# Optimization experiments

Hardware: AMD Instinct MI355X
Metric: run time of the kernel (lower is better)

## Reference

```python
import jax, jax.numpy as jnp
import numpy as np

EMBED = 1024
HEADS = 16
HEAD_DIM = EMBED // HEADS


def setup_inputs() -> dict:
    key = jax.random.key(0)
    ks = jax.random.split(key, 6)
    s = 1.0 / np.sqrt(EMBED)
    return {
        "x": jax.random.normal(ks[0], (2, 2048, EMBED), dtype=jnp.float32),
        "Wq": jax.random.normal(ks[1], (EMBED, EMBED), dtype=jnp.float32) * s,
        "Wk": jax.random.normal(ks[2], (EMBED, EMBED), dtype=jnp.float32) * s,
        "Wv": jax.random.normal(ks[3], (EMBED, EMBED), dtype=jnp.float32) * s,
        "Wfc": jax.random.normal(ks[4], (EMBED, EMBED), dtype=jnp.float32) * s,
        "bfc": jnp.zeros((EMBED,), dtype=jnp.float32),
    }


def reference(x, Wq, Wk, Wv, Wfc, bfc):
    # x: (N, L, E). Linear(E,E,bias=False) applies y = x @ W.T (torch convention).
    N, L, E = x.shape
    q = (x @ Wq.T).reshape(N, L, HEADS, HEAD_DIM)
    k = (x @ Wk.T).reshape(N, L, HEADS, HEAD_DIM)
    v = (x @ Wv.T).reshape(N, L, HEADS, HEAD_DIM)
    # energy: (N, H, Q, K)
    energy = jnp.einsum('nqhd,nkhd->nhqk', q, k)
    # NOTE: original scales by sqrt(embed_size), not sqrt(head_dim)
    attn = jax.nn.softmax(energy / jnp.sqrt(jnp.float32(E)), axis=3)
    out = jnp.einsum('nhql,nlhd->nqhd', attn, v).reshape(N, L, E)
    return out @ Wfc.T + bfc
```

## Files before the change

kernel.cpp:

```cpp
#include <hip/hip_runtime.h>
#include <stdint.h>


typedef short bf16x8 __attribute__((ext_vector_type(8)));
typedef float f32x4 __attribute__((ext_vector_type(4)));

__device__ __forceinline__ unsigned short f2bf(float f) {
  union { float f; unsigned u; } v; v.f = f;
  return (unsigned short)((v.u + 0x7FFFu + ((v.u >> 16) & 1u)) >> 16);
}

#if defined(__has_builtin)
#if __has_builtin(__builtin_amdgcn_cvt_pk_bf16_f32)
#define HAVE_PK_BF16 1
#endif
#if __has_builtin(__builtin_amdgcn_exp2f)
#define EXP2(x) __builtin_amdgcn_exp2f(x)
#endif
#endif
#ifndef EXP2
#define EXP2(x) exp2f(x)
#endif

__device__ __forceinline__ unsigned pk2bf(float a, float b) {
#ifdef HAVE_PK_BF16
  typedef __bf16 bfv2 __attribute__((ext_vector_type(2)));
  union { bfv2 v; unsigned u; } c;
  c.v = __builtin_amdgcn_cvt_pk_bf16_f32(a, b);
  return c.u;
#else
  return (unsigned)f2bf(a) | ((unsigned)f2bf(b) << 16);
#endif
}

__device__ __forceinline__ void load_lds16(const unsigned short* g, unsigned short* l) {
  __builtin_amdgcn_global_load_lds(
      (const __attribute__((address_space(1))) unsigned int*)(const void*)g,
      (__attribute__((address_space(3))) unsigned int*)(void*)l, 16, 0, 0);
}

#define MFMA16(a, b, c) __builtin_amdgcn_mfma_f32_16x16x32_bf16((a), (b), (c), 0, 0, 0)

__global__ __launch_bounds__(256) void cvt_all_kernel(
    const float* __restrict__ x, const float* __restrict__ w0, const float* __restrict__ w1,
    const float* __restrict__ w2, const float* __restrict__ w3, unsigned short* __restrict__ xb,
    unsigned short* __restrict__ d0, unsigned short* __restrict__ d1,
    unsigned short* __restrict__ d2, unsigned short* __restrict__ d3) {
  int i = blockIdx.x * 256 + threadIdx.x;
  const float* s;
  unsigned short* d;
  int off;
  if (i < 1048576) {
    s = x; d = xb; off = i;
  } else {
    int j = i - 1048576;
    int w = j >> 18;
    off = j & 262143;
    s = (w == 0) ? w0 : (w == 1) ? w1 : (w == 2) ? w2 : w3;
    d = (w == 0) ? d0 : (w == 1) ? d1 : (w == 2) ? d2 : d3;
  }
  float4 f = ((const float4*)s)[off];
  uint2 o;
  o.x = pk2bf(f.x, f.y);
  o.y = pk2bf(f.z, f.w);
  ((uint2*)d)[off] = o;
}

__global__ __launch_bounds__(256) void gemm_qkv_kernel(
    const unsigned short* __restrict__ Xb, const unsigned short* __restrict__ Wqb,
    const unsigned short* __restrict__ Wkb, const unsigned short* __restrict__ Wvb,
    unsigned short* __restrict__ Qo, unsigned short* __restrict__ Ko,
    unsigned short* __restrict__ Vt) {
  __shared__ __align__(16) unsigned short As[128 * 32];
  __shared__ __align__(16) unsigned short Bs[128 * 32];
  const int mode = blockIdx.z;
  const unsigned short* W = (mode == 0) ? Wqb : ((mode == 1) ? Wkb : Wvb);
  const int n0 = blockIdx.x * 128;
  const int m0 = blockIdx.y * 128;
  const int tid = threadIdx.x;
  const int lane = tid & 63;
  const int wv = tid >> 6;
  const int wm = (wv >> 1) * 64;
  const int wn = (wv & 1) * 64;
  const int qq = lane >> 4;
  const int cc = lane & 15;

  const f32x4 fz = {0.f, 0.f, 0.f, 0.f};
  f32x4 acc[4][4];
#pragma unroll
  for (int i = 0; i < 4; i++)
#pragma unroll
    for (int j = 0; j < 4; j++) acc[i][j] = fz;

  const int ia0 = tid, ia1 = tid + 256;
  const int ra0 = ia0 >> 2, ca0 = (ia0 & 3) * 8;
  const int ra1 = ia1 >> 2, ca1 = (ia1 & 3) * 8;

  for (int k0 = 0; k0 < 1024; k0 += 32) {
    __syncthreads();
    load_lds16(Xb + (m0 + ra0) * 1024 + k0 + ca0, As + ia0 * 8);
    load_lds16(Xb + (m0 + ra1) * 1024 + k0 + ca1, As + ia1 * 8);
    load_lds16(W + (n0 + ra0) * 1024 + k0 + ca0, Bs + ia0 * 8);
    load_lds16(W + (n0 + ra1) * 1024 + k0 + ca1, Bs + ia1 * 8);
    __syncthreads();
    bf16x8 a[4], b[4];
#pragma unroll
    for (int i = 0; i < 4; i++) a[i] = *(const bf16x8*)(As + (wm + i * 16 + cc) * 32 + qq * 8);
#pragma unroll
    for (int j = 0; j < 4; j++) b[j] = *(const bf16x8*)(Bs + (wn + j * 16 + cc) * 32 + qq * 8);
    if (mode < 2) {
#pragma unroll
      for (int i = 0; i < 4; i++)
#pragma unroll
        for (int j = 0; j < 4; j++) acc[i][j] = MFMA16(b[j], a[i], acc[i][j]);
    } else {
#pragma unroll
      for (int i = 0; i < 4; i++)
#pragma unroll
        for (int j = 0; j < 4; j++) acc[i][j] = MFMA16(a[i], b[j], acc[i][j]);
    }
  }

  if (mode < 2) {
    const float esc = (mode == 0) ? 0.0450842200277801f : 1.0f;
    unsigned short* dst = (mode == 0) ? Qo : Ko;
#pragma unroll
    for (int i = 0; i < 4; i++) {
      int row = m0 + wm + i * 16 + cc;
#pragma unroll
      for (int j = 0; j < 4; j++) {
        int col = n0 + wn + j * 16 + qq * 4;
        uint2 pk;
        pk.x = pk2bf(acc[i][j][0] * esc, acc[i][j][1] * esc);
        pk.y = pk2bf(acc[i][j][2] * esc, acc[i][j][3] * esc);
        *(uint2*)(dst + row * 1024 + col) = pk;
      }
    }
  } else {
#pragma unroll
    for (int i = 0; i < 4; i++)
#pragma unroll
      for (int j = 0; j < 4; j++) {
        int row = m0 + wm + i * 16 + qq * 4;
        int nn = row >> 11, ll = row & 2047;
        int col = n0 + wn + j * 16 + cc;
        int hh = col >> 6, dd = col & 63;
        uint2 pk;
        pk.x = pk2bf(acc[i][j][0], acc[i][j][1]);
        pk.y = pk2bf(acc[i][j][2], acc[i][j][3]);
        *(uint2*)(Vt + ((nn * 16 + hh) * 64 + dd) * 2048 + ll) = pk;
      }
  }
}

__global__ __launch_bounds__(256, 2) void attn_kernel(const unsigned short* __restrict__ Qg,
                                                      const unsigned short* __restrict__ Kg,
                                                      const unsigned short* __restrict__ Vg,
                                                      unsigned short* __restrict__ Og) {
  __shared__ __align__(16) unsigned short Kl[128 * 64];
  __shared__ __align__(16) unsigned short Vl[64 * 128];
  __shared__ __align__(16) unsigned short Pl[4 * 32 * 72];
  const int qt = blockIdx.x, hh = blockIdx.y, nb = blockIdx.z;
  const int tid = threadIdx.x, lane = tid & 63, wv = tid >> 6;
  const int qq = lane >> 4, cc = lane & 15;
  const int q0 = qt * 128 + wv * 32;
  unsigned short* Pw = Pl + wv * (32 * 72);
  const unsigned short* Kbase = Kg + (size_t)(nb * 2048) * 1024 + hh * 64;
  const unsigned short* Vbase = Vg + (size_t)((nb * 16 + hh) * 64) * 2048;

  bf16x8 qf[2][2];
#pragma unroll
  for (int rt = 0; rt < 2; rt++)
#pragma unroll
    for (int kc = 0; kc < 2; kc++)
      qf[rt][kc] = *(const bf16x8*)(Qg + (size_t)(nb * 2048 + q0 + rt * 16 + cc) * 1024 +
                                    hh * 64 + kc * 32 + qq * 8);

  const f32x4 fz = {0.f, 0.f, 0.f, 0.f};
  f32x4 o[2][4];
  float lsum[2] = {0.f, 0.f};
#pragma unroll
  for (int rt = 0; rt < 2; rt++)
#pragma unroll
    for (int vt = 0; vt < 4; vt++) o[rt][vt] = fz;

#pragma unroll 1
  for (int kt = 0; kt < 2048; kt += 128) {
    __syncthreads();
#pragma unroll
    for (int p = 0; p < 4; p++) {
      int idx = p * 256 + tid;
      int r = idx >> 3, c = idx & 7;
      *(bf16x8*)(Kl + r * 64 + ((c ^ (r & 7)) << 3)) =
          *(const bf16x8*)(Kbase + (size_t)(kt + r) * 1024 + c * 8);
    }
#pragma unroll
    for (int p = 0; p < 4; p++) {
      int idx = p * 256 + tid;
      int r = idx >> 4, c = idx & 15;
      *(bf16x8*)(Vl + r * 128 + ((c ^ (r & 15)) << 3)) =
          *(const bf16x8*)(Vbase + (size_t)r * 2048 + kt + c * 8);
    }
    __syncthreads();
#pragma unroll
    for (int hf = 0; hf < 2; hf++) {
      f32x4 s[2][4];
#pragma unroll
      for (int tj = 0; tj < 4; tj++) {
        int row = hf * 64 + tj * 16 + cc;
        const unsigned short* kr = Kl + row * 64;
        int ch0 = (qq ^ (cc & 7)) << 3;
        bf16x8 k0 = *(const bf16x8*)(kr + ch0);
        bf16x8 k1 = *(const bf16x8*)(kr + (ch0 ^ 32));
        f32x4 z0 = fz, z1 = fz;
        z0 = MFMA16(k0, qf[0][0], z0);
        z0 = MFMA16(k1, qf[0][1], z0);
        z1 = MFMA16(k0, qf[1][0], z1);
        z1 = MFMA16(k1, qf[1][1], z1);
        s[0][tj] = z0;
        s[1][tj] = z1;
      }
#pragma unroll
      for (int rt = 0; rt < 2; rt++)
#pragma unroll
        for (int tj = 0; tj < 4; tj++) {
          float p0 = EXP2(s[rt][tj][0]);
          float p1 = EXP2(s[rt][tj][1]);
          float p2 = EXP2(s[rt][tj][2]);
          float p3 = EXP2(s[rt][tj][3]);
          lsum[rt] += (p0 + p1) + (p2 + p3);
          uint2 pk;
          pk.x = pk2bf(p0, p1);
          pk.y = pk2bf(p2, p3);
          *(uint2*)(Pw + (rt * 16 + cc) * 72 + tj * 16 + qq * 4) = pk;
        }
#pragma unroll
      for (int kp = 0; kp < 2; kp++) {
        bf16x8 pf0 = *(const bf16x8*)(Pw + cc * 72 + kp * 32 + qq * 8);
        bf16x8 pf1 = *(const bf16x8*)(Pw + (16 + cc) * 72 + kp * 32 + qq * 8);
        int chb = (hf * 8 + kp * 4 + qq) ^ cc;
#pragma unroll
        for (int vt = 0; vt < 4; vt++) {
          bf16x8 vf = *(const bf16x8*)(Vl + (vt * 16 + cc) * 128 + (chb << 3));
          o[0][vt] = MFMA16(vf, pf0, o[0][vt]);
          o[1][vt] = MFMA16(vf, pf1, o[1][vt]);
        }
      }
    }
  }
#pragma unroll
  for (int rt = 0; rt < 2; rt++) {
    float l = lsum[rt];
    l += __shfl_xor(l, 16);
    l += __shfl_xor(l, 32);
    lsum[rt] = 1.0f / l;
  }
#pragma unroll
  for (int rt = 0; rt < 2; rt++)
#pragma unroll
    for (int vt = 0; vt < 4; vt++) {
      uint2 ov;
      ov.x = pk2bf(o[rt][vt][0] * lsum[rt], o[rt][vt][1] * lsum[rt]);
      ov.y = pk2bf(o[rt][vt][2] * lsum[rt], o[rt][vt][3] * lsum[rt]);
      *(uint2*)(Og + (size_t)(nb * 2048 + q0 + rt * 16 + cc) * 1024 + hh * 64 + vt * 16 +
                qq * 4) = ov;
    }
}

__global__ __launch_bounds__(256) void gemm_fc_kernel(const unsigned short* __restrict__ Ab,
                                                      const unsigned short* __restrict__ Wb,
                                                      const float* __restrict__ bias,
                                                      float* __restrict__ Co) {
  __shared__ __align__(16) unsigned short As[64 * 32];
  __shared__ __align__(16) unsigned short Bs[128 * 32];
  const int n0 = blockIdx.x * 128;
  const int m0 = blockIdx.y * 64;
  const int tid = threadIdx.x;
  const int lane = tid & 63;
  const int wv = tid >> 6;
  const int wm = (wv & 1) * 32;
  const int wn = (wv >> 1) * 64;
  const int qq = lane >> 4;
  const int cc = lane & 15;

  const f32x4 fz = {0.f, 0.f, 0.f, 0.f};
  f32x4 acc[2][4];
#pragma unroll
  for (int i = 0; i < 2; i++)
#pragma unroll
    for (int j = 0; j < 4; j++) acc[i][j] = fz;

  const int raA = tid >> 2, caA = (tid & 3) * 8;
  const int ia0 = tid, ia1 = tid + 256;
  const int rb0 = ia0 >> 2, cb0 = (ia0 & 3) * 8;
  const int rb1 = ia1 >> 2, cb1 = (ia1 & 3) * 8;

  for (int k0 = 0; k0 < 1024; k0 += 32) {
    __syncthreads();
    load_lds16(Ab + (m0 + raA) * 1024 + k0 + caA, As + tid * 8);
    load_lds16(Wb + (n0 + rb0) * 1024 + k0 + cb0, Bs + ia0 * 8);
    load_lds16(Wb + (n0 + rb1) * 1024 + k0 + cb1, Bs + ia1 * 8);
    __syncthreads();
    bf16x8 a[2], b[4];
#pragma unroll
    for (int i = 0; i < 2; i++) a[i] = *(const bf16x8*)(As + (wm + i * 16 + cc) * 32 + qq * 8);
#pragma unroll
    for (int j = 0; j < 4; j++) b[j] = *(const bf16x8*)(Bs + (wn + j * 16 + cc) * 32 + qq * 8);
#pragma unroll
    for (int i = 0; i < 2; i++)
#pragma unroll
      for (int j = 0; j < 4; j++) acc[i][j] = MFMA16(b[j], a[i], acc[i][j]);
  }

#pragma unroll
  for (int i = 0; i < 2; i++) {
    int row = m0 + wm + i * 16 + cc;
#pragma unroll
    for (int j = 0; j < 4; j++) {
      int col = n0 + wn + j * 16 + qq * 4;
      float4 bb = *(const float4*)(bias + col);
      float4 ov;
      ov.x = acc[i][j][0] + bb.x;
      ov.y = acc[i][j][1] + bb.y;
      ov.z = acc[i][j][2] + bb.z;
      ov.w = acc[i][j][3] + bb.w;
      *(float4*)(Co + (size_t)row * 1024 + col) = ov;
    }
  }
}

extern "C" void kernel_launch(void* const* d_in, const int* in_sizes, int n_in, void* d_out,
                              int out_size, void* d_ws, size_t ws_size, hipStream_t stream) {
  const float* x = (const float*)d_in[0];
  const float* Wq = (const float*)d_in[1];
  const float* Wk = (const float*)d_in[2];
  const float* Wv = (const float*)d_in[3];
  const float* Wfc = (const float*)d_in[4];
  const float* bfc = (const float*)d_in[5];
  float* out = (float*)d_out;
  char* ws = (char*)d_ws;
  unsigned short* xb = (unsigned short*)(ws);
  unsigned short* wqb = (unsigned short*)(ws + (8u << 20));
  unsigned short* wkb = (unsigned short*)(ws + (10u << 20));
  unsigned short* wvb = (unsigned short*)(ws + (12u << 20));
  unsigned short* wfb = (unsigned short*)(ws + (14u << 20));
  unsigned short* Qb = (unsigned short*)(ws + (16u << 20));
  unsigned short* Kb = (unsigned short*)(ws + (24u << 20));
  unsigned short* Vtb = (unsigned short*)(ws + (32u << 20));
  unsigned short* Ob = (unsigned short*)(ws + (40u << 20));

  cvt_all_kernel<<<8192, 256, 0, stream>>>(x, Wq, Wk, Wv, Wfc, xb, wqb, wkb, wvb, wfb);
  gemm_qkv_kernel<<<dim3(8, 32, 3), 256, 0, stream>>>(xb, wqb, wkb, wvb, Qb, Kb, Vtb);
  attn_kernel<<<dim3(16, 16, 2), 256, 0, stream>>>(Qb, Kb, Vtb, Ob);
  gemm_fc_kernel<<<dim3(8, 64), 256, 0, stream>>>(Ob, wfb, bfc, out);
}
```

Baseline: 231.3 us.

## Feed softmax probabilities to PV MFMA directly from registers, drop LDS round-trip

The S=K·Q accumulator layout is reused directly as the B operand of a 16x16x16 bf16 MFMA for the P·V product, which removes the per-wave P staging buffer in LDS and its write/read traffic. V fragments are now loaded as 4-element chunks matching that k=16 layout. The cost is twice as many MFMA instructions with half the K depth each, plus narrower LDS reads, in exchange for less LDS use and fewer LDS accesses. Lower LDS use may also allow higher occupancy.

```diff
diff --git a/kernel.cpp b/kernel.cpp
--- a/kernel.cpp
+++ b/kernel.cpp
@@ -3,6 +3,7 @@
 
 
 typedef short bf16x8 __attribute__((ext_vector_type(8)));
+typedef short bf16x4 __attribute__((ext_vector_type(4)));
 typedef float f32x4 __attribute__((ext_vector_type(4)));
 
 __device__ __forceinline__ unsigned short f2bf(float f) {
@@ -40,6 +41,21 @@
 }
 
 #define MFMA16(a, b, c) __builtin_amdgcn_mfma_f32_16x16x32_bf16((a), (b), (c), 0, 0, 0)
+
+#if defined(__has_builtin)
+#if __has_builtin(__builtin_amdgcn_mfma_f32_16x16x16bf16_1k)
+#define MFMAK16(a, b, c) __builtin_amdgcn_mfma_f32_16x16x16bf16_1k((a), (b), (c), 0, 0, 0)
+#elif __has_builtin(__builtin_amdgcn_mfma_f32_16x16x16_bf16)
+#define MFMAK16(a, b, c) __builtin_amdgcn_mfma_f32_16x16x16_bf16((a), (b), (c), 0, 0, 0)
+#endif
+#endif
+#ifndef MFMAK16
+__device__ __forceinline__ f32x4 mfmak16_asm(bf16x4 a, bf16x4 b, f32x4 c) {
+  asm volatile("v_mfma_f32_16x16x16_bf16 %0, %1, %2, %0" : "+v"(c) : "v"(a), "v"(b));
+  return c;
+}
+#define MFMAK16(a, b, c) mfmak16_asm((a), (b), (c))
+#endif
 
 __global__ __launch_bounds__(256) void cvt_all_kernel(
     const float* __restrict__ x, const float* __restrict__ w0, const float* __restrict__ w1,
@@ -159,12 +175,10 @@
                                                       unsigned short* __restrict__ Og) {
   __shared__ __align__(16) unsigned short Kl[128 * 64];
   __shared__ __align__(16) unsigned short Vl[64 * 128];
-  __shared__ __align__(16) unsigned short Pl[4 * 32 * 72];
   const int qt = blockIdx.x, hh = blockIdx.y, nb = blockIdx.z;
   const int tid = threadIdx.x, lane = tid & 63, wv = tid >> 6;
   const int qq = lane >> 4, cc = lane & 15;
   const int q0 = qt * 128 + wv * 32;
-  unsigned short* Pw = Pl + wv * (32 * 72);
   const unsigned short* Kbase = Kg + (size_t)(nb * 2048) * 1024 + hh * 64;
   const unsigned short* Vbase = Vg + (size_t)((nb * 16 + hh) * 64) * 2048;
 
@@ -204,11 +218,9 @@
     __syncthreads();
 #pragma unroll
     for (int hf = 0; hf < 2; hf++) {
-      f32x4 s[2][4];
 #pragma unroll
       for (int tj = 0; tj < 4; tj++) {
-        int row = hf * 64 + tj * 16 + cc;
-        const unsigned short* kr = Kl + row * 64;
+        const unsigned short* kr = Kl + (hf * 64 + tj * 16 + cc) * 64;
         int ch0 = (qq ^ (cc & 7)) << 3;
         bf16x8 k0 = *(const bf16x8*)(kr + ch0);
         bf16x8 k1 = *(const bf16x8*)(kr + (ch0 ^ 32));
@@ -217,33 +229,20 @@
         z0 = MFMA16(k1, qf[0][1], z0);
         z1 = MFMA16(k0, qf[1][0], z1);
         z1 = MFMA16(k1, qf[1][1], z1);
-        s[0][tj] = z0;
-        s[1][tj] = z1;
-      }
-#pragma unroll
-      for (int rt = 0; rt < 2; rt++)
-#pragma unroll
-        for (int tj = 0; tj < 4; tj++) {
-          float p0 = EXP2(s[rt][tj][0]);
-          float p1 = EXP2(s[rt][tj][1]);
-          float p2 = EXP2(s[rt][tj][2]);
-          float p3 = EXP2(s[rt][tj][3]);
-          lsum[rt] += (p0 + p1) + (p2 + p3);
-          uint2 pk;
-          pk.x = pk2bf(p0, p1);
-          pk.y = pk2bf(p2, p3);
-          *(uint2*)(Pw + (rt * 16 + cc) * 72 + tj * 16 + qq * 4) = pk;
-        }
-#pragma unroll
-      for (int kp = 0; kp < 2; kp++) {
-        bf16x8 pf0 = *(const bf16x8*)(Pw + cc * 72 + kp * 32 + qq * 8);
-        bf16x8 pf1 = *(const bf16x8*)(Pw + (16 + cc) * 72 + kp * 32 + qq * 8);
-        int chb = (hf * 8 + kp * 4 + qq) ^ cc;
+        float p00 = EXP2(z0[0]), p01 = EXP2(z0[1]), p02 = EXP2(z0[2]), p03 = EXP2(z0[3]);
+        float p10 = EXP2(z1[0]), p11 = EXP2(z1[1]), p12 = EXP2(z1[2]), p13 = EXP2(z1[3]);
+        lsum[0] += (p00 + p01) + (p02 + p03);
+        lsum[1] += (p10 + p11) + (p12 + p13);
+        union { uint2 u; bf16x4 v; } bp0, bp1;
+        bp0.u.x = pk2bf(p00, p01); bp0.u.y = pk2bf(p02, p03);
+        bp1.u.x = pk2bf(p10, p11); bp1.u.y = pk2bf(p12, p13);
+        int chunk = hf * 8 + tj * 2 + (qq >> 1);
+        int off = (qq & 1) * 4;
 #pragma unroll
         for (int vt = 0; vt < 4; vt++) {
-          bf16x8 vf = *(const bf16x8*)(Vl + (vt * 16 + cc) * 128 + (chb << 3));
-          o[0][vt] = MFMA16(vf, pf0, o[0][vt]);
-          o[1][vt] = MFMA16(vf, pf1, o[1][vt]);
+          bf16x4 vf = *(const bf16x4*)(Vl + (vt * 16 + cc) * 128 + ((chunk ^ cc) << 3) + off);
+          o[0][vt] = MFMAK16(vf, bp0.v, o[0][vt]);
+          o[1][vt] = MFMAK16(vf, bp1.v, o[1][vt]);
         }
       }
     }
```

After: 232.3 us. About the same (+0.4%).
